# Performance work log

Hardware: AMD Instinct MI355X
Metric: run time of the kernel (lower is better)

The kernel has to match this reference:

```python
import jax, jax.numpy as jnp
import numpy as np

N0, N1, N2 = 512, 2048, 8192   # targets, hop1, hop2 node counts
K = 33                          # nneighbor + self loop
IN, HID, OUT, NH = 256, 128, 128, 8
NEG = -9.0e15
ALPHA = 0.2                     # LeakyReLU negative slope


def setup_inputs() -> dict:
    key = jax.random.key(0)
    ks = jax.random.split(key, 8)
    feats = jax.random.normal(ks[0], (N2, IN), jnp.float32)
    # xavier-ish scaled params (gain 1.414)
    W1 = jax.random.normal(ks[1], (NH, IN, HID), jnp.float32) * 0.072
    a1 = jax.random.normal(ks[2], (NH, 2 * HID), jnp.float32) * 0.105
    W2 = jax.random.normal(ks[3], (HID * NH, OUT), jnp.float32) * 0.042
    a2 = jax.random.normal(ks[4], (2 * OUT,), jnp.float32) * 0.105
    # layer1 edges: each of N1 targets gets K distinct neighbors in [0, N2)
    tgt1 = jnp.repeat(jnp.arange(N1, dtype=jnp.int32), K)
    dst1 = ((jnp.arange(N1)[:, None] * 97 + jnp.arange(K)[None, :] * 131) % N2).astype(jnp.int32).reshape(-1)
    src1 = jax.random.randint(ks[5], (N1 * K,), 0, N2, jnp.int32)
    # layer2 edges: each of N0 targets gets K distinct neighbors in [0, N1)
    tgt2 = jnp.repeat(jnp.arange(N0, dtype=jnp.int32), K)
    dst2 = ((jnp.arange(N0)[:, None] * 53 + jnp.arange(K)[None, :] * 61) % N1).astype(jnp.int32).reshape(-1)
    src2 = jax.random.randint(ks[6], (N0 * K,), 0, N1, jnp.int32)
    return dict(feats=feats, W1=W1, a1=a1, W2=W2, a2=a2,
                src1=src1, dst1=dst1, tgt1=tgt1, src2=src2, dst2=dst2, tgt2=tgt2)


def gat_layer(x, W, a, src, dst, tgt, t_len):
    # x: [n, in], W: [in, d], a: [2d]
    h = x @ W                                   # [n, d]
    d = h.shape[1]
    # concat([h[src], h[dst]]) @ a  ==  h[src]@a[:d] + h[dst]@a[d:]
    e = h[src] @ a[:d] + h[dst] @ a[d:]         # [E]
    e = jnp.where(e > 0, e, ALPHA * e)          # LeakyReLU
    att = jnp.full((t_len, h.shape[0]), NEG, h.dtype).at[tgt, dst].set(e)
    att = jax.nn.softmax(att, axis=1)           # dense row softmax (masked entries ~0)
    return jax.nn.elu(att @ h)                  # [t_len, d]


def reference(feats, W1, a1, W2, a2, src1, dst1, tgt1, src2, dst2, tgt2):
    # layer 1: nhead independent GAT heads over hop2 features
    heads = jax.vmap(lambda W, a: gat_layer(feats, W, a, src1, dst1, tgt1, N1))(W1, a1)  # [NH, N1, HID]
    x = jnp.transpose(heads, (1, 0, 2)).reshape(N1, NH * HID)  # torch.cat(dim=1)
    # layer 2: single GAT layer producing [N0, OUT]
    return gat_layer(x, W2, a2, src2, dst2, tgt2, N0)
```

## Files before the change

### kernel.cpp

```cpp
#include <hip/hip_runtime.h>
#include <math.h>

#define ALPHA 0.2f

constexpr int CN0 = 512, CN1 = 2048, CN2 = 8192, CK = 33;
constexpr int CIN = 256, CHID = 128, CNH = 8;

using u16    = unsigned short;
using f32x4  = __attribute__((ext_vector_type(4))) float;
using bf16x8 = __attribute__((ext_vector_type(8))) short;
using short8 = __attribute__((ext_vector_type(8))) short;

__device__ __forceinline__ u16 f2bf(float f) {
    unsigned u = __float_as_uint(f);
    u += 0x7fff + ((u >> 16) & 1);
    return (u16)(u >> 16);
}
__device__ __forceinline__ float bf2f(u16 h) {
    return __uint_as_float(((unsigned)h) << 16);
}

#define GLD16(g, l)                                                        \
    __builtin_amdgcn_global_load_lds(                                      \
        (const __attribute__((address_space(1))) void*)(g),                \
        (__attribute__((address_space(3))) void*)(l), 16, 0, 0)

__global__ __launch_bounds__(256) void prep_k(const float* __restrict__ feats,
                                              u16* __restrict__ fb,
                                              const float* __restrict__ W1,
                                              u16* __restrict__ w1t,
                                              const float* __restrict__ W2,
                                              u16* __restrict__ w2t) {
    __shared__ float t[32][33];
    int b = blockIdx.x;
    if (b < 2048) {
        const int i = (b * 256 + threadIdx.x) * 4;
        const float4 v = *reinterpret_cast<const float4*>(feats + i);
        *reinterpret_cast<ushort4*>(fb + i) =
            make_ushort4(f2bf(v.x), f2bf(v.y), f2bf(v.z), f2bf(v.w));
        return;
    }
    b -= 2048;
    const float* ip;
    u16* op;
    int R, C, r0, c0;
    if (b < 256) {
        const int h = b >> 5, w = b & 31;
        ip = W1 + (size_t)h * CIN * CHID;
        op = w1t + (size_t)h * CIN * CHID;
        R = CIN; C = CHID; r0 = (w >> 2) * 32; c0 = (w & 3) * 32;
    } else {
        b -= 256;
        ip = W2; op = w2t;
        R = CNH * CHID; C = CHID; r0 = (b >> 2) * 32; c0 = (b & 3) * 32;
    }
    const int tx = threadIdx.x & 31, ty = threadIdx.x >> 5;
#pragma unroll
    for (int i = 0; i < 4; ++i)
        t[ty + 8 * i][tx] = ip[(size_t)(r0 + ty + 8 * i) * C + c0 + tx];
    __syncthreads();
#pragma unroll
    for (int i = 0; i < 4; ++i)
        op[(size_t)(c0 + ty + 8 * i) * R + r0 + tx] = f2bf(t[tx][ty + 8 * i]);
}

template <int KSTEPS, bool BF16OUT, bool SCORES>
__global__ __launch_bounds__(256) void gemm_mfma(const u16* __restrict__ A, int lda,
                                                 const u16* __restrict__ Bt, int ldb,
                                                 u16* __restrict__ Cb,
                                                 float* __restrict__ Cf, int ldc,
                                                 long csplit,
                                                 const float* __restrict__ av,
                                                 float* __restrict__ s1o,
                                                 float* __restrict__ s2o,
                                                 int snodes) {
    constexpr int SMEMSZ = BF16OUT ? (128 * 136 * 2) : 32768;
    __shared__ __attribute__((aligned(16))) char smem[SMEMSZ];

    const int tid  = threadIdx.x;
    const int lane = tid & 63;
    const int wave = tid >> 6;
    const int row0 = blockIdx.y * 128;
    const int col0 = blockIdx.x * 128;
    const int kbase = blockIdx.z * (KSTEPS * 32);
    const int wr = (wave >> 1) * 64;
    const int wc = (wave & 1) * 64;

    f32x4 acc[4][4];
#pragma unroll
    for (int m = 0; m < 4; ++m)
#pragma unroll
        for (int n = 0; n < 4; ++n) acc[m][n] = (f32x4){0.f, 0.f, 0.f, 0.f};

    const int r0c = tid >> 2;
    const int cs0 = tid & 3;
    const int c0  = (cs0 - (r0c >> 1)) & 3;
    const int r1c = r0c + 64;

    const u16* ga0 = A + (size_t)(row0 + r0c) * lda + kbase + c0 * 8;
    const u16* ga1 = A + (size_t)(row0 + r1c) * lda + kbase + c0 * 8;
    const u16* gb0 = Bt + (size_t)(col0 + r0c) * ldb + kbase + c0 * 8;
    const u16* gb1 = Bt + (size_t)(col0 + r1c) * ldb + kbase + c0 * 8;

    auto STAGE = [&](int s) {
        const int k0 = s * 32;
        char* base = smem + (s & 1) * 16384;
        u16* as = (u16*)base + wave * 512;
        u16* bs = (u16*)(base + 8192) + wave * 512;
        GLD16(ga0 + k0, as);
        GLD16(ga1 + k0, as + 2048);
        GLD16(gb0 + k0, bs);
        GLD16(gb1 + k0, bs + 2048);
    };

    STAGE(0);
    __syncthreads();

    for (int s = 0; s < KSTEPS; ++s) {
        if (s + 1 < KSTEPS) STAGE(s + 1);

        const u16* Acur = (const u16*)(smem + (s & 1) * 16384);
        const u16* Bcur = Acur + 4096;

        bf16x8 af[4], bfr[4];
#pragma unroll
        for (int m = 0; m < 4; ++m) {
            const int rt = wr + m * 16 + (lane & 15);
            const int cs = ((lane >> 4) + (rt >> 1)) & 3;
            af[m] = *reinterpret_cast<const bf16x8*>(Acur + rt * 32 + cs * 8);
            const int rt2 = wc + m * 16 + (lane & 15);
            const int cs2 = ((lane >> 4) + (rt2 >> 1)) & 3;
            bfr[m] = *reinterpret_cast<const bf16x8*>(Bcur + rt2 * 32 + cs2 * 8);
        }
#pragma unroll
        for (int m = 0; m < 4; ++m)
#pragma unroll
            for (int n = 0; n < 4; ++n)
                acc[m][n] = __builtin_amdgcn_mfma_f32_16x16x32_bf16(
                    af[m], bfr[n], acc[m][n], 0, 0, 0);

        __syncthreads();
    }

    if constexpr (BF16OUT) {
        u16* Cs = (u16*)smem;
#pragma unroll
        for (int m = 0; m < 4; ++m) {
            const int rr = wr + m * 16 + (lane >> 4) * 4;
#pragma unroll
            for (int n = 0; n < 4; ++n) {
                const int cc = wc + n * 16 + (lane & 15);
#pragma unroll
                for (int q = 0; q < 4; ++q)
                    Cs[(rr + q) * 136 + cc] = f2bf(acc[m][n][q]);
            }
        }
        __syncthreads();
#pragma unroll
        for (int i = 0; i < 8; ++i) {
            const int cid = i * 256 + tid;
            const int r  = cid >> 4;
            const int kc = cid & 15;
            const int4 v = *reinterpret_cast<const int4*>(&Cs[r * 136 + kc * 8]);
            *reinterpret_cast<int4*>(&Cb[(long)(row0 + r) * ldc + col0 + kc * 8]) = v;
        }
    } else {
        const long cbase = (long)blockIdx.z * csplit;
#pragma unroll
        for (int m = 0; m < 4; ++m) {
            const int rr = row0 + wr + m * 16 + (lane >> 4) * 4;
#pragma unroll
            for (int n = 0; n < 4; ++n) {
                const int cc = col0 + wc + n * 16 + (lane & 15);
#pragma unroll
                for (int q = 0; q < 4; ++q)
                    Cf[cbase + (long)(rr + q) * ldc + cc] = acc[m][n][q];
            }
        }
    }

    if constexpr (SCORES) {
        __shared__ float sred1[2][128];
        __shared__ float sred2[2][128];
        const int head = blockIdx.x;
        float av1[4], av2[4];
#pragma unroll
        for (int n = 0; n < 4; ++n) {
            const int c = wc + n * 16 + (lane & 15);
            av1[n] = av[head * 2 * CHID + c];
            av2[n] = av[head * 2 * CHID + CHID + c];
        }
        float p1[4][4], p2[4][4];
#pragma unroll
        for (int m = 0; m < 4; ++m)
#pragma unroll
            for (int q = 0; q < 4; ++q) {
                float t1 = 0.f, t2 = 0.f;
#pragma unroll
                for (int n = 0; n < 4; ++n) {
                    t1 = fmaf(acc[m][n][q], av1[n], t1);
                    t2 = fmaf(acc[m][n][q], av2[n], t2);
                }
#pragma unroll
                for (int mk = 1; mk < 16; mk <<= 1) {
                    t1 += __shfl_xor(t1, mk);
                    t2 += __shfl_xor(t2, mk);
                }
                p1[m][q] = t1;
                p2[m][q] = t2;
            }
        if ((lane & 15) == 0) {
            const int g = lane >> 4;
#pragma unroll
            for (int m = 0; m < 4; ++m)
#pragma unroll
                for (int q = 0; q < 4; ++q) {
                    sred1[wave & 1][wr + m * 16 + g * 4 + q] = p1[m][q];
                    sred2[wave & 1][wr + m * 16 + g * 4 + q] = p2[m][q];
                }
        }
        __syncthreads();
        if (tid < 128) {
            s1o[head * snodes + row0 + tid] = sred1[0][tid] + sred1[1][tid];
            s2o[head * snodes + row0 + tid] = sred2[0][tid] + sred2[1][tid];
        }
    }
}

__global__ __launch_bounds__(128) void agg1_k(const float* __restrict__ s1,
                                              const float* __restrict__ s2,
                                              const int* __restrict__ src,
                                              const int* __restrict__ dst,
                                              const u16* __restrict__ hm,
                                              u16* __restrict__ xout) {
    __shared__ float wgt[CNH][CK];
    __shared__ int dsts[CK];

    const int t    = blockIdx.x;
    const int tid  = threadIdx.x;
    const int wv   = tid >> 6;
    const int lane = tid & 63;

    int sv = 0, dv = 0;
    if (lane < CK) {
        sv = src[t * CK + lane];
        dv = dst[t * CK + lane];
        if (tid < CK) dsts[tid] = dv;
    }
#pragma unroll
    for (int hh = 0; hh < 4; ++hh) {
        const int head = wv * 4 + hh;
        float e = -3.0e38f;
        if (lane < CK) {
            const float ee = s1[head * CN2 + sv] + s2[head * CN2 + dv];
            e = (ee > 0.f) ? ee : ALPHA * ee;
        }
        float m = e;
#pragma unroll
        for (int mm = 1; mm < 64; mm <<= 1) m = fmaxf(m, __shfl_xor(m, mm));
        const float p = (lane < CK) ? __expf(e - m) : 0.f;
        float s = p;
#pragma unroll
        for (int mm = 1; mm < 64; mm <<= 1) s += __shfl_xor(s, mm);
        if (lane < CK) wgt[head][lane] = p / s;
    }
    __syncthreads();

    const int c0   = tid * 8;
    const int head = tid >> 4;
    float acc[8] = {0.f, 0.f, 0.f, 0.f, 0.f, 0.f, 0.f, 0.f};
#pragma unroll
    for (int k = 0; k < CK; ++k) {
        const short8 hv = *reinterpret_cast<const short8*>(
            hm + (size_t)dsts[k] * (CNH * CHID) + c0);
        const float w = wgt[head][k];
#pragma unroll
        for (int j = 0; j < 8; ++j) acc[j] = fmaf(w, bf2f((u16)hv[j]), acc[j]);
    }
    short8 o;
#pragma unroll
    for (int j = 0; j < 8; ++j) {
        const float v = (acc[j] > 0.f) ? acc[j] : __expf(acc[j]) - 1.f;
        o[j] = (short)f2bf(v);
    }
    *reinterpret_cast<short8*>(xout + (size_t)t * (CNH * CHID) + c0) = o;
}

__global__ __launch_bounds__(256) void scores2_k(const float* __restrict__ part,
                                                 const float* __restrict__ a,
                                                 float* __restrict__ h2,
                                                 float* __restrict__ s1,
                                                 float* __restrict__ s2) {
    const int wid  = (blockIdx.x * 256 + threadIdx.x) >> 6;
    const int lane = threadIdx.x & 63;
    const int j = lane * 2;
    float x0 = 0.f, x1 = 0.f;
#pragma unroll
    for (int sp = 0; sp < 8; ++sp) {
        const float2 v = *reinterpret_cast<const float2*>(
            part + (size_t)sp * CN1 * CHID + (size_t)wid * CHID + j);
        x0 += v.x; x1 += v.y;
    }
    *reinterpret_cast<float2*>(h2 + (size_t)wid * CHID + j) = make_float2(x0, x1);
    float d1 = x0 * a[j] + x1 * a[j + 1];
    float d2 = x0 * a[CHID + j] + x1 * a[CHID + j + 1];
#pragma unroll
    for (int m = 1; m < 64; m <<= 1) {
        d1 += __shfl_xor(d1, m);
        d2 += __shfl_xor(d2, m);
    }
    if (lane == 0) { s1[wid] = d1; s2[wid] = d2; }
}

__global__ __launch_bounds__(256) void agg2_k(const float* __restrict__ s1,
                                              const float* __restrict__ s2,
                                              const int* __restrict__ src,
                                              const int* __restrict__ dst,
                                              const float* __restrict__ h2,
                                              float* __restrict__ out) {
    const int t    = (blockIdx.x * 256 + threadIdx.x) >> 6;
    const int lane = threadIdx.x & 63;

    float e = -3.0e38f;
    int dv = 0;
    if (lane < CK) {
        const int sv = src[t * CK + lane];
        dv = dst[t * CK + lane];
        const float ee = s1[sv] + s2[dv];
        e = (ee > 0.f) ? ee : ALPHA * ee;
    }
    float m = e;
#pragma unroll
    for (int mm = 1; mm < 64; mm <<= 1) m = fmaxf(m, __shfl_xor(m, mm));
    float p = (lane < CK) ? __expf(e - m) : 0.f;
    float ssum = p;
#pragma unroll
    for (int mm = 1; mm < 64; mm <<= 1) ssum += __shfl_xor(ssum, mm);
    const float invs = 1.f / ssum;

    float a0 = 0.f, a1 = 0.f;
#pragma unroll
    for (int k = 0; k < CK; ++k) {
        const float w = __shfl(p, k) * invs;
        const int d = __shfl(dv, k);
        const float2 hv = *reinterpret_cast<const float2*>(h2 + (size_t)d * CHID + lane * 2);
        a0 = fmaf(w, hv.x, a0);
        a1 = fmaf(w, hv.y, a1);
    }
    a0 = (a0 > 0.f) ? a0 : __expf(a0) - 1.f;
    a1 = (a1 > 0.f) ? a1 : __expf(a1) - 1.f;
    *reinterpret_cast<float2*>(out + (size_t)t * CHID + lane * 2) = make_float2(a0, a1);
}

extern "C" void kernel_launch(void* const* d_in, const int* in_sizes, int n_in,
                              void* d_out, int out_size, void* d_ws, size_t ws_size,
                              hipStream_t stream) {
    const float* feats = (const float*)d_in[0];
    const float* W1    = (const float*)d_in[1];
    const float* a1    = (const float*)d_in[2];
    const float* W2    = (const float*)d_in[3];
    const float* a2    = (const float*)d_in[4];
    const int*   src1  = (const int*)d_in[5];
    const int*   dst1  = (const int*)d_in[6];
    const int*   src2  = (const int*)d_in[8];
    const int*   dst2  = (const int*)d_in[9];
    float* out = (float*)d_out;

    char* w = (char*)d_ws;
    u16*   fb   = (u16*)w;                 w += (size_t)CN2 * CIN * 2;
    u16*   w1t  = (u16*)w;                 w += (size_t)CNH * CIN * CHID * 2;
    u16*   w2t  = (u16*)w;                 w += (size_t)CNH * CHID * CHID * 2;
    u16*   h1b  = (u16*)w;                 w += (size_t)CN2 * CNH * CHID * 2;
    float* s1   = (float*)w;               w += (size_t)CNH * CN2 * 4;
    float* s2   = (float*)w;               w += (size_t)CNH * CN2 * 4;
    u16*   xb   = (u16*)w;                 w += (size_t)CN1 * CNH * CHID * 2;
    float* part = (float*)w;               w += (size_t)8 * CN1 * CHID * 4;
    float* h2   = (float*)w;               w += (size_t)CN1 * CHID * 4;
    float* s21  = (float*)w;               w += (size_t)CN1 * 4;
    float* s22  = (float*)w;               w += (size_t)CN1 * 4;

    prep_k<<<dim3(2048 + 256 + 128), 256, 0, stream>>>(feats, fb, W1, w1t, W2, w2t);

    gemm_mfma<8, true, true><<<dim3((CNH * CHID) / 128, CN2 / 128), 256, 0, stream>>>(
        fb, CIN, w1t, CIN, h1b, nullptr, CNH * CHID, 0, a1, s1, s2, CN2);

    agg1_k<<<dim3(CN1), 128, 0, stream>>>(s1, s2, src1, dst1, h1b, xb);

    gemm_mfma<4, false, false><<<dim3(1, CN1 / 128, 8), 256, 0, stream>>>(
        xb, CNH * CHID, w2t, CNH * CHID, nullptr, part, CHID, (long)CN1 * CHID,
        nullptr, nullptr, nullptr, 0);

    scores2_k<<<dim3(CN1 / 4), 256, 0, stream>>>(part, a2, h2, s21, s22);

    agg2_k<<<dim3(CN0 / 4), 256, 0, stream>>>(s21, s22, src2, dst2, h2, out);
}
```

Before: 61.22 us.

## Reassociate layer-1 GAT: aggregate raw features first, then project per head

Attention scores are now computed as feats·(W1·a1) using precomputed per-head vectors, so the full 8192x1024 hidden projection is no longer needed for scoring. Raw bf16 features of neighbors are aggregated per head into a [NH, N1, IN] buffer, and a head-split MFMA GEMM with fused ELU then projects only the N1 target rows. This replaces the large hop-2 GEMM with a GEMM over the 2048 hop-1 targets. The cost is an extra intermediate buffer, a separate score kernel, and a change in rounding order, since aggregation now happens in bf16 before the projection.

```diff
diff --git a/kernel.cpp b/kernel.cpp
--- a/kernel.cpp
+++ b/kernel.cpp
@@ -30,7 +30,9 @@
                                               const float* __restrict__ W1,
                                               u16* __restrict__ w1t,
                                               const float* __restrict__ W2,
-                                              u16* __restrict__ w2t) {
+                                              u16* __restrict__ w2t,
+                                              const float* __restrict__ a1,
+                                              float* __restrict__ pvec) {
     __shared__ float t[32][33];
     int b = blockIdx.x;
     if (b < 2048) {
@@ -38,6 +40,18 @@
         const float4 v = *reinterpret_cast<const float4*>(feats + i);
         *reinterpret_cast<ushort4*>(fb + i) =
             make_ushort4(f2bf(v.x), f2bf(v.y), f2bf(v.z), f2bf(v.w));
+        return;
+    }
+    if (b >= 2432) {
+        const int i = b - 2432;
+        const int h = i >> 1, half = i & 1;
+        const int j = threadIdx.x;
+        const float* wrow = W1 + (size_t)h * CIN * CHID + (size_t)j * CHID;
+        const float* ah   = a1 + h * 2 * CHID + half * CHID;
+        float d = 0.f;
+#pragma unroll 8
+        for (int c = 0; c < CHID; ++c) d = fmaf(wrow[c], ah[c], d);
+        pvec[(h * 2 + half) * CIN + j] = d;
         return;
     }
     b -= 2048;
@@ -64,16 +78,101 @@
         op[(size_t)(c0 + ty + 8 * i) * R + r0 + tx] = f2bf(t[tx][ty + 8 * i]);
 }
 
-template <int KSTEPS, bool BF16OUT, bool SCORES>
+__global__ __launch_bounds__(256) void sgemm1_k(const u16* __restrict__ fb,
+                                                const float* __restrict__ pvec,
+                                                float* __restrict__ s1,
+                                                float* __restrict__ s2) {
+    const int node = (blockIdx.x * 256 + threadIdx.x) >> 6;
+    const int lane = threadIdx.x & 63;
+    const ushort4 hv = *reinterpret_cast<const ushort4*>(fb + (size_t)node * CIN + lane * 4);
+    const float v0 = bf2f(hv.x), v1 = bf2f(hv.y), v2 = bf2f(hv.z), v3 = bf2f(hv.w);
+#pragma unroll
+    for (int h = 0; h < CNH; ++h) {
+        const float4 p1 = *reinterpret_cast<const float4*>(pvec + (h * 2 + 0) * CIN + lane * 4);
+        const float4 p2 = *reinterpret_cast<const float4*>(pvec + (h * 2 + 1) * CIN + lane * 4);
+        float d1 = v0 * p1.x + v1 * p1.y + v2 * p1.z + v3 * p1.w;
+        float d2 = v0 * p2.x + v1 * p2.y + v2 * p2.z + v3 * p2.w;
+#pragma unroll
+        for (int m = 1; m < 64; m <<= 1) {
+            d1 += __shfl_xor(d1, m);
+            d2 += __shfl_xor(d2, m);
+        }
+        if (lane == 0) {
+            s1[h * CN2 + node] = d1;
+            s2[h * CN2 + node] = d2;
+        }
+    }
+}
+
+__global__ __launch_bounds__(128) void agg1g_k(const float* __restrict__ s1,
+                                               const float* __restrict__ s2,
+                                               const int* __restrict__ src,
+                                               const int* __restrict__ dst,
+                                               const u16* __restrict__ fb,
+                                               u16* __restrict__ gb) {
+    __shared__ float wgt[CNH][CK];
+    __shared__ int dsts[CK];
+
+    const int t    = blockIdx.x;
+    const int tid  = threadIdx.x;
+    const int wv   = tid >> 6;
+    const int lane = tid & 63;
+
+    int sv = 0, dv = 0;
+    if (lane < CK) {
+        sv = src[t * CK + lane];
+        dv = dst[t * CK + lane];
+        if (tid < CK) dsts[tid] = dv;
+    }
+#pragma unroll
+    for (int hh = 0; hh < 4; ++hh) {
+        const int head = wv * 4 + hh;
+        float e = -3.0e38f;
+        if (lane < CK) {
+            const float ee = s1[head * CN2 + sv] + s2[head * CN2 + dv];
+            e = (ee > 0.f) ? ee : ALPHA * ee;
+        }
+        float m = e;
+#pragma unroll
+        for (int mm = 1; mm < 64; mm <<= 1) m = fmaxf(m, __shfl_xor(m, mm));
+        const float p = (lane < CK) ? __expf(e - m) : 0.f;
+        float s = p;
+#pragma unroll
+        for (int mm = 1; mm < 64; mm <<= 1) s += __shfl_xor(s, mm);
+        if (lane < CK) wgt[head][lane] = p / s;
+    }
+    __syncthreads();
+
+    const int c2 = tid * 2;
+    float acc[CNH][2];
+#pragma unroll
+    for (int h = 0; h < CNH; ++h) { acc[h][0] = 0.f; acc[h][1] = 0.f; }
+#pragma unroll 4
+    for (int k = 0; k < CK; ++k) {
+        const unsigned w2 = *reinterpret_cast<const unsigned*>(
+            fb + (size_t)dsts[k] * CIN + c2);
+        const float f0 = bf2f((u16)(w2 & 0xffff));
+        const float f1 = bf2f((u16)(w2 >> 16));
+#pragma unroll
+        for (int h = 0; h < CNH; ++h) {
+            const float wk = wgt[h][k];
+            acc[h][0] = fmaf(wk, f0, acc[h][0]);
+            acc[h][1] = fmaf(wk, f1, acc[h][1]);
+        }
+    }
+#pragma unroll
+    for (int h = 0; h < CNH; ++h) {
+        const unsigned o = ((unsigned)f2bf(acc[h][1]) << 16) | f2bf(acc[h][0]);
+        *reinterpret_cast<unsigned*>(gb + ((size_t)h * CN1 + t) * CIN + c2) = o;
+    }
+}
+
+template <int KSTEPS, bool BF16OUT, bool ELUOUT, bool HEADSPLIT>
 __global__ __launch_bounds__(256) void gemm_mfma(const u16* __restrict__ A, int lda,
                                                  const u16* __restrict__ Bt, int ldb,
                                                  u16* __restrict__ Cb,
                                                  float* __restrict__ Cf, int ldc,
-                                                 long csplit,
-                                                 const float* __restrict__ av,
-                                                 float* __restrict__ s1o,
-                                                 float* __restrict__ s2o,
-                                                 int snodes) {
+                                                 long csplit) {
     constexpr int SMEMSZ = BF16OUT ? (128 * 136 * 2) : 32768;
     __shared__ __attribute__((aligned(16))) char smem[SMEMSZ];
 
@@ -81,8 +180,17 @@
     const int lane = tid & 63;
     const int wave = tid >> 6;
     const int row0 = blockIdx.y * 128;
-    const int col0 = blockIdx.x * 128;
-    const int kbase = blockIdx.z * (KSTEPS * 32);
+
+    int kbase, bcol0, ccol0;
+    if constexpr (HEADSPLIT) {
+        A  += (size_t)blockIdx.z * CN1 * CIN;
+        Bt += (size_t)blockIdx.z * CHID * CIN;
+        kbase = 0; bcol0 = 0; ccol0 = blockIdx.z * CHID;
+    } else {
+        kbase = blockIdx.z * (KSTEPS * 32);
+        bcol0 = blockIdx.x * 128;
+        ccol0 = bcol0;
+    }
     const int wr = (wave >> 1) * 64;
     const int wc = (wave & 1) * 64;
 
@@ -99,8 +207,8 @@
 
     const u16* ga0 = A + (size_t)(row0 + r0c) * lda + kbase + c0 * 8;
     const u16* ga1 = A + (size_t)(row0 + r1c) * lda + kbase + c0 * 8;
-    const u16* gb0 = Bt + (size_t)(col0 + r0c) * ldb + kbase + c0 * 8;
-    const u16* gb1 = Bt + (size_t)(col0 + r1c) * ldb + kbase + c0 * 8;
+    const u16* gb0 = Bt + (size_t)(bcol0 + r0c) * ldb + kbase + c0 * 8;
+    const u16* gb1 = Bt + (size_t)(bcol0 + r1c) * ldb + kbase + c0 * 8;
 
     auto STAGE = [&](int s) {
         const int k0 = s * 32;
@@ -151,8 +259,11 @@
             for (int n = 0; n < 4; ++n) {
                 const int cc = wc + n * 16 + (lane & 15);
 #pragma unroll
-                for (int q = 0; q < 4; ++q)
-                    Cs[(rr + q) * 136 + cc] = f2bf(acc[m][n][q]);
+                for (int q = 0; q < 4; ++q) {
+                    float v = acc[m][n][q];
+                    if (ELUOUT) v = (v > 0.f) ? v : __expf(v) - 1.f;
+                    Cs[(rr + q) * 136 + cc] = f2bf(v);
+                }
             }
         }
         __syncthreads();
@@ -162,128 +273,22 @@
             const int r  = cid >> 4;
             const int kc = cid & 15;
             const int4 v = *reinterpret_cast<const int4*>(&Cs[r * 136 + kc * 8]);
-            *reinterpret_cast<int4*>(&Cb[(long)(row0 + r) * ldc + col0 + kc * 8]) = v;
+            *reinterpret_cast<int4*>(&Cb[(long)(row0 + r) * ldc + ccol0 + kc * 8]) = v;
         }
     } else {
-        const long cbase = (long)blockIdx.z * csplit;
+        const long cbase = HEADSPLIT ? 0 : (long)blockIdx.z * csplit;
 #pragma unroll
         for (int m = 0; m < 4; ++m) {
             const int rr = row0 + wr + m * 16 + (lane >> 4) * 4;
 #pragma unroll
             for (int n = 0; n < 4; ++n) {
-                const int cc = col0 + wc + n * 16 + (lane & 15);
+                const int cc = ccol0 + wc + n * 16 + (lane & 15);
 #pragma unroll
                 for (int q = 0; q < 4; ++q)
                     Cf[cbase + (long)(rr + q) * ldc + cc] = acc[m][n][q];
             }
         }
     }
-
-    if constexpr (SCORES) {
-        __shared__ float sred1[2][128];
-        __shared__ float sred2[2][128];
-        const int head = blockIdx.x;
-        float av1[4], av2[4];
-#pragma unroll
-        for (int n = 0; n < 4; ++n) {
-            const int c = wc + n * 16 + (lane & 15);
-            av1[n] = av[head * 2 * CHID + c];
-            av2[n] = av[head * 2 * CHID + CHID + c];
-        }
-        float p1[4][4], p2[4][4];
-#pragma unroll
-        for (int m = 0; m < 4; ++m)
-#pragma unroll
-            for (int q = 0; q < 4; ++q) {
-                float t1 = 0.f, t2 = 0.f;
-#pragma unroll
-                for (int n = 0; n < 4; ++n) {
-                    t1 = fmaf(acc[m][n][q], av1[n], t1);
-                    t2 = fmaf(acc[m][n][q], av2[n], t2);
-                }
-#pragma unroll
-                for (int mk = 1; mk < 16; mk <<= 1) {
-                    t1 += __shfl_xor(t1, mk);
-                    t2 += __shfl_xor(t2, mk);
-                }
-                p1[m][q] = t1;
-                p2[m][q] = t2;
-            }
-        if ((lane & 15) == 0) {
-            const int g = lane >> 4;
-#pragma unroll
-            for (int m = 0; m < 4; ++m)
-#pragma unroll
-                for (int q = 0; q < 4; ++q) {
-                    sred1[wave & 1][wr + m * 16 + g * 4 + q] = p1[m][q];
-                    sred2[wave & 1][wr + m * 16 + g * 4 + q] = p2[m][q];
-                }
-        }
-        __syncthreads();
-        if (tid < 128) {
-            s1o[head * snodes + row0 + tid] = sred1[0][tid] + sred1[1][tid];
-            s2o[head * snodes + row0 + tid] = sred2[0][tid] + sred2[1][tid];
-        }
-    }
-}
-
-__global__ __launch_bounds__(128) void agg1_k(const float* __restrict__ s1,
-                                              const float* __restrict__ s2,
-                                              const int* __restrict__ src,
-                                              const int* __restrict__ dst,
-                                              const u16* __restrict__ hm,
-                                              u16* __restrict__ xout) {
-    __shared__ float wgt[CNH][CK];
-    __shared__ int dsts[CK];
-
-    const int t    = blockIdx.x;
-    const int tid  = threadIdx.x;
-    const int wv   = tid >> 6;
-    const int lane = tid & 63;
-
-    int sv = 0, dv = 0;
-    if (lane < CK) {
-        sv = src[t * CK + lane];
-        dv = dst[t * CK + lane];
-        if (tid < CK) dsts[tid] = dv;
-    }
-#pragma unroll
-    for (int hh = 0; hh < 4; ++hh) {
-        const int head = wv * 4 + hh;
-        float e = -3.0e38f;
-        if (lane < CK) {
-            const float ee = s1[head * CN2 + sv] + s2[head * CN2 + dv];
-            e = (ee > 0.f) ? ee : ALPHA * ee;
-        }
-        float m = e;
-#pragma unroll
-        for (int mm = 1; mm < 64; mm <<= 1) m = fmaxf(m, __shfl_xor(m, mm));
-        const float p = (lane < CK) ? __expf(e - m) : 0.f;
-        float s = p;
-#pragma unroll
-        for (int mm = 1; mm < 64; mm <<= 1) s += __shfl_xor(s, mm);
-        if (lane < CK) wgt[head][lane] = p / s;
-    }
-    __syncthreads();
-
-    const int c0   = tid * 8;
-    const int head = tid >> 4;
-    float acc[8] = {0.f, 0.f, 0.f, 0.f, 0.f, 0.f, 0.f, 0.f};
-#pragma unroll
-    for (int k = 0; k < CK; ++k) {
-        const short8 hv = *reinterpret_cast<const short8*>(
-            hm + (size_t)dsts[k] * (CNH * CHID) + c0);
-        const float w = wgt[head][k];
-#pragma unroll
-        for (int j = 0; j < 8; ++j) acc[j] = fmaf(w, bf2f((u16)hv[j]), acc[j]);
-    }
-    short8 o;
-#pragma unroll
-    for (int j = 0; j < 8; ++j) {
-        const float v = (acc[j] > 0.f) ? acc[j] : __expf(acc[j]) - 1.f;
-        o[j] = (short)f2bf(v);
-    }
-    *reinterpret_cast<short8*>(xout + (size_t)t * (CNH * CHID) + c0) = o;
 }
 
 __global__ __launch_bounds__(256) void scores2_k(const float* __restrict__ part,
@@ -370,25 +375,28 @@
     u16*   fb   = (u16*)w;                 w += (size_t)CN2 * CIN * 2;
     u16*   w1t  = (u16*)w;                 w += (size_t)CNH * CIN * CHID * 2;
     u16*   w2t  = (u16*)w;                 w += (size_t)CNH * CHID * CHID * 2;
-    u16*   h1b  = (u16*)w;                 w += (size_t)CN2 * CNH * CHID * 2;
+    float* pvec = (float*)w;               w += (size_t)CNH * 2 * CIN * 4;
     float* s1   = (float*)w;               w += (size_t)CNH * CN2 * 4;
     float* s2   = (float*)w;               w += (size_t)CNH * CN2 * 4;
+    u16*   gb   = (u16*)w;                 w += (size_t)CNH * CN1 * CIN * 2;
     u16*   xb   = (u16*)w;                 w += (size_t)CN1 * CNH * CHID * 2;
     float* part = (float*)w;               w += (size_t)8 * CN1 * CHID * 4;
     float* h2   = (float*)w;               w += (size_t)CN1 * CHID * 4;
     float* s21  = (float*)w;               w += (size_t)CN1 * 4;
     float* s22  = (float*)w;               w += (size_t)CN1 * 4;
 
-    prep_k<<<dim3(2048 + 256 + 128), 256, 0, stream>>>(feats, fb, W1, w1t, W2, w2t);
-
-    gemm_mfma<8, true, true><<<dim3((CNH * CHID) / 128, CN2 / 128), 256, 0, stream>>>(
-        fb, CIN, w1t, CIN, h1b, nullptr, CNH * CHID, 0, a1, s1, s2, CN2);
-
-    agg1_k<<<dim3(CN1), 128, 0, stream>>>(s1, s2, src1, dst1, h1b, xb);
-
-    gemm_mfma<4, false, false><<<dim3(1, CN1 / 128, 8), 256, 0, stream>>>(
-        xb, CNH * CHID, w2t, CNH * CHID, nullptr, part, CHID, (long)CN1 * CHID,
-        nullptr, nullptr, nullptr, 0);
+    prep_k<<<dim3(2048 + 256 + 128 + 16), 256, 0, stream>>>(
+        feats, fb, W1, w1t, W2, w2t, a1, pvec);
+
+    sgemm1_k<<<dim3(CN2 / 4), 256, 0, stream>>>(fb, pvec, s1, s2);
+
+    agg1g_k<<<dim3(CN1), 128, 0, stream>>>(s1, s2, src1, dst1, fb, gb);
+
+    gemm_mfma<8, true, true, true><<<dim3(1, CN1 / 128, CNH), 256, 0, stream>>>(
+        gb, CIN, w1t, CIN, xb, nullptr, CNH * CHID, 0);
+
+    gemm_mfma<4, false, false, false><<<dim3(1, CN1 / 128, 8), 256, 0, stream>>>(
+        xb, CNH * CHID, w2t, CNH * CHID, nullptr, part, CHID, (long)CN1 * CHID);
 
     scores2_k<<<dim3(CN1 / 4), 256, 0, stream>>>(part, a2, h2, s21, s22);
 
```

Result: faster. 57.74 us (-5.7%).
